# Optimization experiments

Hardware: AMD Instinct MI355X
Metric: run time of the kernel (lower is better)

The kernel has to match this reference:

```python
import jax, jax.numpy as jnp
import numpy as np

N = 8192        # batch_size == num nodes == num hyperedges
D = 512         # hidden_dim
H_HEADS = 8
HD = D // H_HEADS
TOP_K = 16
EPS = 1e-5      # LayerNorm eps


def setup_inputs() -> dict:
    key = jax.random.key(0)
    ks = jax.random.split(key, 10)
    def rn(k, shape, scale=0.02):
        return jax.random.normal(k, shape, dtype=jnp.float32) * scale
    return {
        "x0": jax.random.normal(ks[0], (N, D), dtype=jnp.float32),
        "x1": jax.random.normal(ks[1], (N, D), dtype=jnp.float32),
        # modality projections: Linear -> ReLU -> LayerNorm (per modality)
        "w_p0": rn(ks[2], (D, D)), "b_p0": jnp.zeros((D,), jnp.float32),
        "g0": jnp.ones((D,), jnp.float32), "beta0": jnp.zeros((D,), jnp.float32),
        "w_p1": rn(ks[3], (D, D)), "b_p1": jnp.zeros((D,), jnp.float32),
        "g1": jnp.ones((D,), jnp.float32), "beta1": jnp.zeros((D,), jnp.float32),
        # MultiheadAttention packed in-proj + out-proj
        "in_w": rn(ks[4], (3 * D, D)), "in_b": jnp.zeros((3 * D,), jnp.float32),
        "out_w": rn(ks[5], (D, D)), "out_b": jnp.zeros((D,), jnp.float32),
        # edge weight predictor MLP
        "ew_w1": rn(ks[6], (D // 2, D)), "ew_b1": jnp.zeros((D // 2,), jnp.float32),
        "ew_w2": rn(ks[7], (1, D // 2)), "ew_b2": jnp.zeros((1,), jnp.float32),
    }


def _layernorm(x, g, b):
    m = x.mean(-1, keepdims=True)
    v = ((x - m) ** 2).mean(-1, keepdims=True)
    return (x - m) * jax.lax.rsqrt(v + EPS) * g + b


def _forward(x0, x1, w_p0, b_p0, g0, beta0, w_p1, b_p1, g1, beta1,
             in_w, in_b, out_w, out_b, ew_w1, ew_b1, ew_w2, ew_b2):
    # per-modality projection: Linear -> ReLU -> LayerNorm
    p0 = _layernorm(jax.nn.relu(x0 @ w_p0.T + b_p0), g0, beta0)
    p1 = _layernorm(jax.nn.relu(x1 @ w_p1.T + b_p1), g1, beta1)
    seq = jnp.stack([p0, p1], axis=1)                       # [N, 2, D]
    # cross-modal MHA (self-attention over the 2 modality tokens)
    qkv = seq @ in_w.T + in_b                               # [N, 2, 3D]
    q, k, v = jnp.split(qkv, 3, axis=-1)
    q = q.reshape(N, 2, H_HEADS, HD)
    k = k.reshape(N, 2, H_HEADS, HD)
    v = v.reshape(N, 2, H_HEADS, HD)
    scores = jnp.einsum('bqhd,bkhd->bhqk', q, k) / jnp.sqrt(jnp.float32(HD))
    attn = jax.nn.softmax(scores, axis=-1)                  # [N, h, 2, 2]
    ctx = jnp.einsum('bhqk,bkhd->bqhd', attn, v).reshape(N, 2, D)
    attended = ctx @ out_w.T + out_b                        # [N, 2, D]
    fused = attended.mean(axis=1)                           # [N, D]
    # node-node attention similarity, row-softmax
    sim = jax.nn.softmax(fused @ fused.T, axis=1)           # [N, N]
    _, idx = jax.lax.top_k(sim, TOP_K)                      # [N, K]
    vals = jnp.take_along_axis(sim, idx, axis=1)            # [N, K]
    rows = jnp.arange(N)
    # H[i,i]=1 first, then H[neighbor, i] = sim[i, neighbor] (may overwrite diag)
    H = jnp.zeros((N, N), sim.dtype).at[rows, rows].set(1.0)
    H = H.at[idx, rows[:, None]].set(vals)
    colsum = H.sum(axis=0)
    H = H.at[rows, rows].set(jnp.where(colsum == 0, 1.0, H[rows, rows]))
    # edge weights
    hidden = jax.nn.relu(fused @ ew_w1.T + ew_b1)
    ew = jax.nn.sigmoid(hidden @ ew_w2.T + ew_b2)[:, 0]     # [N]
    ew = jnp.maximum(ew, 1e-8)
    return H, ew


def reference(x0, x1, w_p0, b_p0, g0, beta0, w_p1, b_p1, g1, beta1,
              in_w, in_b, out_w, out_b, ew_w1, ew_b1, ew_w2, ew_b2):
    return _forward(x0, x1, w_p0, b_p0, g0, beta0, w_p1, b_p1, g1, beta1,
                    in_w, in_b, out_w, out_b, ew_w1, ew_b1, ew_w2, ew_b2)
```

## Files before the change

### kernel.cpp

```cpp
#include <hip/hip_runtime.h>
#include <hip/hip_bf16.h>

#define NN 8192
#define DD 512

typedef unsigned short u16;
typedef __bf16 bf16_t;
typedef bf16_t bf16x8 __attribute__((ext_vector_type(8)));
typedef float f32x4 __attribute__((ext_vector_type(4)));

__device__ __forceinline__ float bf2f(u16 h) {
    union { unsigned u; float f; } v; v.u = ((unsigned)h) << 16; return v.f;
}
__device__ __forceinline__ float bflo(unsigned u) {
    union { unsigned u; float f; } v; v.u = u << 16; return v.f;
}
__device__ __forceinline__ float bfhi(unsigned u) {
    union { unsigned u; float f; } v; v.u = u & 0xFFFF0000u; return v.f;
}
__device__ __forceinline__ u16 f2bf(float f) {
    union { float f; unsigned u; } v; v.f = f;
    unsigned r = v.u + 0x7fffu + ((v.u >> 16) & 1u);
    return (u16)(r >> 16);
}

#define PIPE_BARRIER(N) do { \
    __builtin_amdgcn_sched_barrier(0); \
    asm volatile("s_waitcnt vmcnt(" #N ")" ::: "memory"); \
    __builtin_amdgcn_s_barrier(); \
    __builtin_amdgcn_sched_barrier(0); \
} while (0)

__global__ __launch_bounds__(256) void cvt5(
        const float* __restrict__ s0, u16* __restrict__ d0,
        const float* __restrict__ s1, u16* __restrict__ d1,
        const float* __restrict__ s2, u16* __restrict__ d2,
        const float* __restrict__ s3, u16* __restrict__ d3,
        const float* __restrict__ s4, u16* __restrict__ d4) {
    size_t v = ((size_t)blockIdx.x * 256 + threadIdx.x) * 8;
    const float* s; u16* d; size_t off;
    if (v < 262144)       { s = s0; d = d0; off = v; }
    else if (v < 524288)  { s = s1; d = d1; off = v - 262144; }
    else if (v < 1310720) { s = s2; d = d2; off = v - 524288; }
    else if (v < 1572864) { s = s3; d = d3; off = v - 1310720; }
    else                  { s = s4; d = d4; off = v - 1572864; }
    float4 a = *(const float4*)(s + off);
    float4 b = *(const float4*)(s + off + 4);
    ushort4 o0 = make_ushort4(f2bf(a.x), f2bf(a.y), f2bf(a.z), f2bf(a.w));
    ushort4 o1 = make_ushort4(f2bf(b.x), f2bf(b.y), f2bf(b.z), f2bf(b.w));
    *(ushort4*)(d + off) = o0;
    *(ushort4*)(d + off + 4) = o1;
}

#define EPS_LDS 136
__global__ __launch_bounds__(256) void gemm_proj(
        const float* __restrict__ X0, const float* __restrict__ X1,
        const u16* __restrict__ B0, const float* __restrict__ bias0,
        const u16* __restrict__ B1, const float* __restrict__ bias1,
        u16* __restrict__ C) {
    __shared__ alignas(16) u16 Smem[2][16384];
    const int t = threadIdx.x;
    const int lane = t & 63;
    const int wave = t >> 6;
    const int wm = (wave >> 1) * 64;
    const int wn = (wave & 1) * 64;
    const int rowA = blockIdx.y * 128;
    const int rowB = blockIdx.x * 128;
    const bool mod1 = (int)blockIdx.y >= 64;
    const float* A32 = mod1 ? X1 + (size_t)(rowA - 8192) * DD
                            : X0 + (size_t)rowA * DD;
    const u16* B = mod1 ? B1 : B0;
    const float* bias = mod1 ? bias1 : bias0;

    f32x4 acc[4][4] = {};
    const int mrow = lane & 15;
    const int kk = (lane >> 4) * 8;
    const int trow = t >> 3;
    const int koff = (t & 7) * 8;

    float ar[4][8];
    auto LOADA = [&](int k0) {
        #pragma unroll
        for (int r = 0; r < 4; ++r) {
            const float* s = A32 + (size_t)(r * 32 + trow) * DD + k0 + koff;
            float4 f0 = *(const float4*)s;
            float4 f1 = *(const float4*)(s + 4);
            ar[r][0] = f0.x; ar[r][1] = f0.y; ar[r][2] = f0.z; ar[r][3] = f0.w;
            ar[r][4] = f1.x; ar[r][5] = f1.y; ar[r][6] = f1.z; ar[r][7] = f1.w;
        }
    };
    auto WRITEA = [&](int buf) {
        u16* As = Smem[buf];
        #pragma unroll
        for (int r = 0; r < 4; ++r) {
            int chunk = r * 256 + t;
            ushort4 o0 = make_ushort4(f2bf(ar[r][0]), f2bf(ar[r][1]),
                                      f2bf(ar[r][2]), f2bf(ar[r][3]));
            ushort4 o1 = make_ushort4(f2bf(ar[r][4]), f2bf(ar[r][5]),
                                      f2bf(ar[r][6]), f2bf(ar[r][7]));
            *(ushort4*)(As + chunk * 8) = o0;
            *(ushort4*)(As + chunk * 8 + 4) = o1;
        }
    };
    auto BSTAGE = [&](int buf, int k0) {
        u16* Bs = Smem[buf] + 8192;
        #pragma unroll
        for (int r = 0; r < 4; ++r) {
            int chunk = r * 256 + t;
            const u16* srcB = B + (size_t)(rowB + (chunk >> 3)) * DD + k0 + (chunk & 7) * 8;
            __builtin_amdgcn_global_load_lds(
                (const __attribute__((address_space(1))) void*)srcB,
                (__attribute__((address_space(3))) void*)(Bs + chunk * 8), 16, 0, 0);
        }
    };

    LOADA(0); BSTAGE(0, 0); WRITEA(0);
    __syncthreads();
    int cur = 0;
    for (int ti = 0; ti < 8; ++ti) {
        if (ti < 7) { LOADA((ti + 1) << 6); BSTAGE(cur ^ 1, (ti + 1) << 6); }
        const u16* As = Smem[cur];
        const u16* Bs = Smem[cur] + 8192;
        #pragma unroll
        for (int ks = 0; ks < 64; ks += 32) {
            bf16x8 af[4], bfv[4];
            #pragma unroll
            for (int i = 0; i < 4; ++i)
                af[i] = *(const bf16x8*)(As + (wm + i * 16 + mrow) * 64 + ks + kk);
            #pragma unroll
            for (int j = 0; j < 4; ++j)
                bfv[j] = *(const bf16x8*)(Bs + (wn + j * 16 + mrow) * 64 + ks + kk);
            #pragma unroll
            for (int i = 0; i < 4; ++i)
                #pragma unroll
                for (int j = 0; j < 4; ++j)
                    acc[i][j] = __builtin_amdgcn_mfma_f32_16x16x32_bf16(af[i], bfv[j], acc[i][j], 0, 0, 0);
        }
        if (ti < 7) WRITEA(cur ^ 1);
        __syncthreads();
        cur ^= 1;
    }

    u16* Ep = &Smem[0][0];
    const int er0 = wm + (lane >> 4) * 4;
    const int ec0 = wn + (lane & 15);
    #pragma unroll
    for (int j = 0; j < 4; ++j) {
        int c = ec0 + j * 16;
        float bv = bias[rowB + c];
        #pragma unroll
        for (int i = 0; i < 4; ++i) {
            #pragma unroll
            for (int r = 0; r < 4; ++r) {
                float v = fmaxf(acc[i][j][r] + bv, 0.0f);
                Ep[(er0 + i * 16 + r) * EPS_LDS + c] = f2bf(v);
            }
        }
    }
    __syncthreads();
    #pragma unroll
    for (int pass = 0; pass < 8; ++pass) {
        int chunk = pass * 256 + t;
        int rloc = chunk >> 4, coff = (chunk & 15) * 8;
        bf16x8 v = *(const bf16x8*)(Ep + rloc * EPS_LDS + coff);
        *(bf16x8*)(C + (size_t)(rowA + rloc) * DD + rowB + coff) = v;
    }
}

__global__ __launch_bounds__(256) void gemm_qkv(const u16* __restrict__ A,
        const u16* __restrict__ B, const float* __restrict__ bias,
        u16* __restrict__ V, float* __restrict__ AL) {
    __shared__ alignas(16) u16 Smem[3][8192];
    const int t = threadIdx.x;
    const int lane = t & 63;
    const int wave = t >> 6;
    const int wm = (wave >> 1) * 64;
    const int wn = (wave & 1) * 64;
    const int c = blockIdx.x;
    const int rowA = blockIdx.y * 128;
    const bool isQK = (c < 8);

    f32x4 acc[4][4] = {};
    const int mrow = lane & 15;
    const int kk = (lane >> 4) * 8;

    auto STAGE = [&](int buf, int k0) {
        u16* As = Smem[buf];
        u16* Bs = Smem[buf] + 4096;
        #pragma unroll
        for (int r = 0; r < 2; ++r) {
            int chunk = r * 256 + t;
            int rr = chunk >> 2;
            int ko = (chunk & 3) * 8;
            int brow = isQK ? (c * 64 + rr + ((rr >= 64) ? 448 : 0))
                            : (1024 + (c - 8) * 128 + rr);
            const u16* srcA = A + (size_t)(rowA + rr) * DD + k0 + ko;
            __builtin_amdgcn_global_load_lds(
                (const __attribute__((address_space(1))) void*)srcA,
                (__attribute__((address_space(3))) void*)(As + chunk * 8), 16, 0, 0);
            const u16* srcB = B + (size_t)brow * DD + k0 + ko;
            __builtin_amdgcn_global_load_lds(
                (const __attribute__((address_space(1))) void*)srcB,
                (__attribute__((address_space(3))) void*)(Bs + chunk * 8), 16, 0, 0);
        }
    };
    auto COMPUTE = [&](int buf) {
        const u16* As = Smem[buf];
        const u16* Bs = Smem[buf] + 4096;
        bf16x8 af[4], bfv[4];
        #pragma unroll
        for (int i = 0; i < 4; ++i)
            af[i] = *(const bf16x8*)(As + (wm + i * 16 + mrow) * 32 + kk);
        #pragma unroll
        for (int j = 0; j < 4; ++j)
            bfv[j] = *(const bf16x8*)(Bs + (wn + j * 16 + mrow) * 32 + kk);
        #pragma unroll
        for (int i = 0; i < 4; ++i)
            #pragma unroll
            for (int j = 0; j < 4; ++j)
                acc[i][j] = __builtin_amdgcn_mfma_f32_16x16x32_bf16(af[i], bfv[j], acc[i][j], 0, 0, 0);
    };

    STAGE(0, 0);
    STAGE(1, 32);
    PIPE_BARRIER(4);
    #pragma unroll
    for (int ts = 0; ts < 14; ++ts) {
        STAGE((ts + 2) % 3, (ts + 2) * 32);
        COMPUTE(ts % 3);
        PIPE_BARRIER(4);
    }
    COMPUTE(2);
    PIPE_BARRIER(0);
    COMPUTE(0);
    __syncthreads();

    u16* Ep = &Smem[0][0];
    const int er0 = wm + (lane >> 4) * 4;
    const int ec0 = wn + (lane & 15);
    #pragma unroll
    for (int j = 0; j < 4; ++j) {
        int cc = ec0 + j * 16;
        int bcol = isQK ? ((cc < 64) ? c * 64 + cc : 448 + c * 64 + cc)
                        : (1024 + (c - 8) * 128 + cc);
        float bv = bias[bcol];
        #pragma unroll
        for (int i = 0; i < 4; ++i) {
            #pragma unroll
            for (int r = 0; r < 4; ++r)
                Ep[(er0 + i * 16 + r) * EPS_LDS + cc] = f2bf(acc[i][j][r] + bv);
        }
    }
    __syncthreads();
    if (isQK) {
        int nd = t >> 2, cb = t & 3, tt2 = cb >> 1, ss = cb & 1;
        const u16* qrow = Ep + (2 * nd + tt2) * EPS_LDS;
        const u16* krow = Ep + (2 * nd + ss) * EPS_LDS + 64;
        float s = 0.0f;
        #pragma unroll
        for (int d8 = 0; d8 < 8; ++d8) {
            bf16x8 qv = *(const bf16x8*)(qrow + d8 * 8);
            bf16x8 kv = *(const bf16x8*)(krow + d8 * 8);
            #pragma unroll
            for (int u = 0; u < 8; ++u) s += (float)qv[u] * (float)kv[u];
        }
        s *= 0.125f;
        float o = __shfl_xor(s, 1);
        float mm = fmaxf(s, o);
        float es = __expf(s - mm), eo = __expf(o - mm);
        float a = es / (es + eo);
        float a2 = __shfl_xor(a, 2);
        float al = 0.5f * (a + a2);
        if (cb < 2)
            AL[(size_t)(rowA / 2 + nd) * 16 + c * 2 + cb] = al;
    } else {
        #pragma unroll
        for (int pass = 0; pass < 8; ++pass) {
            int chunk = pass * 256 + t;
            int rloc = chunk >> 4, coff = (chunk & 15) * 8;
            bf16x8 v = *(const bf16x8*)(Ep + rloc * EPS_LDS + coff);
            *(bf16x8*)(V + (size_t)(rowA + rloc) * 512 + (c - 8) * 128 + coff) = v;
        }
    }
}

__global__ __launch_bounds__(256) void gemm_outp(
        const float* __restrict__ AL, const u16* __restrict__ V,
        const u16* __restrict__ W, const float* __restrict__ bias,
        u16* __restrict__ C) {
    __shared__ alignas(16) u16 Smem[2][16384];
    const int t = threadIdx.x;
    const int lane = t & 63;
    const int wave = t >> 6;
    const int wm = (wave >> 1) * 64;
    const int wn = (wave & 1) * 64;
    const int rowA = blockIdx.y * 128;
    const int rowB = blockIdx.x * 128;

    f32x4 acc[4][4] = {};
    const int mrow = lane & 15;
    const int kk = (lane >> 4) * 8;
    const int trow = t >> 3;
    const int koff = (t & 7) * 8;

    uint4 v0r[4], v1r[4];
    float2 alr[4];
    auto LOADA = [&](int ti) {
        #pragma unroll
        for (int r = 0; r < 4; ++r) {
            int node = rowA + r * 32 + trow;
            alr[r] = *(const float2*)(AL + (size_t)node * 16 + ti * 2);
            const u16* v0p = V + (size_t)(2 * node) * 512 + ti * 64 + koff;
            v0r[r] = *(const uint4*)v0p;
            v1r[r] = *(const uint4*)(v0p + 512);
        }
    };
    auto WRITEA = [&](int buf) {
        u16* As = Smem[buf];
        #pragma unroll
        for (int r = 0; r < 4; ++r) {
            int chunk = r * 256 + t;
            union { u16 us[8]; ushort4 u4[2]; } o;
            #pragma unroll
            for (int q = 0; q < 4; ++q) {
                unsigned w0 = (&v0r[r].x)[q], w1 = (&v1r[r].x)[q];
                o.us[q * 2]     = f2bf(alr[r].x * bflo(w0) + alr[r].y * bflo(w1));
                o.us[q * 2 + 1] = f2bf(alr[r].x * bfhi(w0) + alr[r].y * bfhi(w1));
            }
            *(ushort4*)(As + chunk * 8) = o.u4[0];
            *(ushort4*)(As + chunk * 8 + 4) = o.u4[1];
        }
    };
    auto BSTAGE = [&](int buf, int k0) {
        u16* Bs = Smem[buf] + 8192;
        #pragma unroll
        for (int r = 0; r < 4; ++r) {
            int chunk = r * 256 + t;
            const u16* srcB = W + (size_t)(rowB + (chunk >> 3)) * DD + k0 + (chunk & 7) * 8;
            __builtin_amdgcn_global_load_lds(
                (const __attribute__((address_space(1))) void*)srcB,
                (__attribute__((address_space(3))) void*)(Bs + chunk * 8), 16, 0, 0);
        }
    };

    LOADA(0); BSTAGE(0, 0); WRITEA(0);
    __syncthreads();
    int cur = 0;
    for (int ti = 0; ti < 8; ++ti) {
        if (ti < 7) { LOADA(ti + 1); BSTAGE(cur ^ 1, (ti + 1) << 6); }
        const u16* As = Smem[cur];
        const u16* Bs = Smem[cur] + 8192;
        #pragma unroll
        for (int ks = 0; ks < 64; ks += 32) {
            bf16x8 af[4], bfv[4];
            #pragma unroll
            for (int i = 0; i < 4; ++i)
                af[i] = *(const bf16x8*)(As + (wm + i * 16 + mrow) * 64 + ks + kk);
            #pragma unroll
            for (int j = 0; j < 4; ++j)
                bfv[j] = *(const bf16x8*)(Bs + (wn + j * 16 + mrow) * 64 + ks + kk);
            #pragma unroll
            for (int i = 0; i < 4; ++i)
                #pragma unroll
                for (int j = 0; j < 4; ++j)
                    acc[i][j] = __builtin_amdgcn_mfma_f32_16x16x32_bf16(af[i], bfv[j], acc[i][j], 0, 0, 0);
        }
        if (ti < 7) WRITEA(cur ^ 1);
        __syncthreads();
        cur ^= 1;
    }

    u16* Ep = &Smem[0][0];
    const int er0 = wm + (lane >> 4) * 4;
    const int ec0 = wn + (lane & 15);
    #pragma unroll
    for (int j = 0; j < 4; ++j) {
        int c = ec0 + j * 16;
        float bv = bias[rowB + c];
        #pragma unroll
        for (int i = 0; i < 4; ++i) {
            #pragma unroll
            for (int r = 0; r < 4; ++r)
                Ep[(er0 + i * 16 + r) * EPS_LDS + c] = f2bf(acc[i][j][r] + bv);
        }
    }
    __syncthreads();
    #pragma unroll
    for (int pass = 0; pass < 8; ++pass) {
        int chunk = pass * 256 + t;
        int rloc = chunk >> 4, coff = (chunk & 15) * 8;
        bf16x8 v = *(const bf16x8*)(Ep + rloc * EPS_LDS + coff);
        *(bf16x8*)(C + (size_t)(rowA + rloc) * DD + rowB + coff) = v;
    }
}

#define SYM_LDS 129
__global__ __launch_bounds__(256) void gemm_symh(const u16* __restrict__ F,
        u16* __restrict__ C, const u16* __restrict__ W1,
        const float* __restrict__ b1, u16* __restrict__ Hid) {
    __shared__ alignas(16) u16 Smem[3][8192];
    const int bx = blockIdx.x, by = blockIdx.y;
    const bool isHid = (bx >= 64);
    if (!isHid && bx < by) return;
    const int t = threadIdx.x;
    const int lane = t & 63;
    const int wave = t >> 6;
    const int wm = (wave >> 1) * 64;
    const int wn = (wave & 1) * 64;
    const int rowI = by * 128;
    const int rowJ = isHid ? (bx - 64) * 128 : bx * 128;
    const u16* Bsrc = isHid ? W1 : F;

    f32x4 acc[4][4] = {};
    const int mrow = lane & 15;
    const int kk = (lane >> 4) * 8;

    auto STAGE = [&](int buf, int k0) {
        u16* As = Smem[buf];
        u16* Bs = Smem[buf] + 4096;
        #pragma unroll
        for (int r = 0; r < 2; ++r) {
            int chunk = r * 256 + t;
            int row = chunk >> 2;
            int ko = (chunk & 3) * 8;
            const u16* srcA = F + (size_t)(rowI + row) * DD + k0 + ko;
            __builtin_amdgcn_global_load_lds(
                (const __attribute__((address_space(1))) void*)srcA,
                (__attribute__((address_space(3))) void*)(As + chunk * 8), 16, 0, 0);
            const u16* srcB = Bsrc + (size_t)(rowJ + row) * DD + k0 + ko;
            __builtin_amdgcn_global_load_lds(
                (const __attribute__((address_space(1))) void*)srcB,
                (__attribute__((address_space(3))) void*)(Bs + chunk * 8), 16, 0, 0);
        }
    };
    auto COMPUTE = [&](int buf) {
        const u16* As = Smem[buf];
        const u16* Bs = Smem[buf] + 4096;
        bf16x8 af[4], bfv[4];
        #pragma unroll
        for (int i = 0; i < 4; ++i)
            af[i] = *(const bf16x8*)(As + (wm + i * 16 + mrow) * 32 + kk);
        #pragma unroll
        for (int j = 0; j < 4; ++j)
            bfv[j] = *(const bf16x8*)(Bs + (wn + j * 16 + mrow) * 32 + kk);
        #pragma unroll
        for (int i = 0; i < 4; ++i)
            #pragma unroll
            for (int j = 0; j < 4; ++j)
                acc[i][j] = __builtin_amdgcn_mfma_f32_16x16x32_bf16(af[i], bfv[j], acc[i][j], 0, 0, 0);
    };

    STAGE(0, 0);
    STAGE(1, 32);
    PIPE_BARRIER(4);
    #pragma unroll
    for (int ts = 0; ts < 14; ++ts) {
        STAGE((ts + 2) % 3, (ts + 2) * 32);
        COMPUTE(ts % 3);
        PIPE_BARRIER(4);
    }
    COMPUTE(2);
    PIPE_BARRIER(0);
    COMPUTE(0);
    __syncthreads();

    u16* Ep = &Smem[0][0];
    const int er0 = wm + (lane >> 4) * 4;
    const int ec0 = wn + (lane & 15);
    #pragma unroll
    for (int j = 0; j < 4; ++j) {
        int c = ec0 + j * 16;
        float bv = isHid ? b1[rowJ + c] : 0.0f;
        #pragma unroll
        for (int i = 0; i < 4; ++i) {
            #pragma unroll
            for (int r = 0; r < 4; ++r) {
                float v = acc[i][j][r] + bv;
                if (isHid) v = fmaxf(v, 0.0f);
                Ep[(er0 + i * 16 + r) * SYM_LDS + c] = f2bf(v);
            }
        }
    }
    __syncthreads();
    if (isHid) {
        #pragma unroll
        for (int pass = 0; pass < 8; ++pass) {
            int chunk = pass * 256 + t;
            int rloc = chunk >> 4, coff = (chunk & 15) * 8;
            union { u16 us[8]; bf16x8 v; } buf;
            #pragma unroll
            for (int k = 0; k < 8; ++k) buf.us[k] = Ep[rloc * SYM_LDS + coff + k];
            *(bf16x8*)(Hid + (size_t)(rowI + rloc) * 256 + rowJ + coff) = buf.v;
        }
        return;
    }
    #pragma unroll
    for (int pass = 0; pass < 8; ++pass) {
        int chunk = pass * 256 + t;
        int rloc = chunk >> 4, coff = (chunk & 15) * 8;
        union { u16 us[8]; bf16x8 v; } buf;
        #pragma unroll
        for (int k = 0; k < 8; ++k) buf.us[k] = Ep[rloc * SYM_LDS + coff + k];
        *(bf16x8*)(C + (size_t)(rowI + rloc) * NN + rowJ + coff) = buf.v;
    }
    if (bx != by) {
        #pragma unroll
        for (int pass = 0; pass < 8; ++pass) {
            int chunk = pass * 256 + t;
            int tr = chunk >> 4, roff = (chunk & 15) * 8;
            union { u16 us[8]; bf16x8 v; } buf;
            #pragma unroll
            for (int k = 0; k < 8; ++k) buf.us[k] = Ep[(roff + k) * SYM_LDS + tr];
            *(bf16x8*)(C + (size_t)(rowJ + tr) * NN + rowI + roff) = buf.v;
        }
    }
}

__global__ __launch_bounds__(256) void ln2_kernel(const u16* __restrict__ y,
        const float* __restrict__ g0, const float* __restrict__ b0,
        const float* __restrict__ g1, const float* __restrict__ b1,
        u16* __restrict__ seq) {
    int n = blockIdx.x * 4 + (threadIdx.x >> 6);
    int lane = threadIdx.x & 63;
    int modality = n >> 13, node = n & (NN - 1);
    const float* g = modality ? g1 : g0;
    const float* b = modality ? b1 : b0;
    bf16x8 v = *(const bf16x8*)(y + (size_t)n * DD + lane * 8);
    float x[8];
    float s = 0.0f;
    #pragma unroll
    for (int u = 0; u < 8; ++u) { x[u] = (float)v[u]; s += x[u]; }
    #pragma unroll
    for (int off = 32; off; off >>= 1) s += __shfl_xor(s, off);
    float mean = s * (1.0f / DD);
    float vs = 0.0f;
    #pragma unroll
    for (int u = 0; u < 8; ++u) { x[u] -= mean; vs += x[u] * x[u]; }
    #pragma unroll
    for (int off = 32; off; off >>= 1) vs += __shfl_xor(vs, off);
    float inv = rsqrtf(vs * (1.0f / DD) + 1e-5f);
    float4 ga = *(const float4*)(g + lane * 8);
    float4 gb = *(const float4*)(g + lane * 8 + 4);
    float4 ba = *(const float4*)(b + lane * 8);
    float4 bb = *(const float4*)(b + lane * 8 + 4);
    union { u16 us[8]; bf16x8 v; } o;
    o.us[0] = f2bf(x[0] * inv * ga.x + ba.x);
    o.us[1] = f2bf(x[1] * inv * ga.y + ba.y);
    o.us[2] = f2bf(x[2] * inv * ga.z + ba.z);
    o.us[3] = f2bf(x[3] * inv * ga.w + ba.w);
    o.us[4] = f2bf(x[4] * inv * gb.x + bb.x);
    o.us[5] = f2bf(x[5] * inv * gb.y + bb.y);
    o.us[6] = f2bf(x[6] * inv * gb.z + bb.z);
    o.us[7] = f2bf(x[7] * inv * gb.w + bb.w);
    *(bf16x8*)(seq + (size_t)node * (2 * DD) + modality * DD + lane * 8) = o.v;
}

__global__ __launch_bounds__(256) void topk_bf16(u16* __restrict__ S,
        float* __restrict__ topv, int* __restrict__ topi,
        u16* __restrict__ hidden, const float* __restrict__ w2,
        const float* __restrict__ b2, float* __restrict__ ew_out,
        float* __restrict__ H) {
    const int blk = blockIdx.x;
    const int t = threadIdx.x;
    const float4 z4 = make_float4(0.f, 0.f, 0.f, 0.f);
    if (blk >= 2048) {
        int wv = t >> 6, lane = t & 63;
        int n0 = (blk - 2048) * 64 + wv * 16;
        float wa = w2[lane], wb = w2[lane + 64], wc = w2[lane + 128], wd = w2[lane + 192];
        for (int q = 0; q < 16; ++q) {
            int n = n0 + q;
            const u16* hr = hidden + (size_t)n * 256;
            float s = bf2f(hr[lane]) * wa + bf2f(hr[lane + 64]) * wb
                    + bf2f(hr[lane + 128]) * wc + bf2f(hr[lane + 192]) * wd;
            #pragma unroll
            for (int off = 32; off; off >>= 1) s += __shfl_xor(s, off);
            if (lane == 0) {
                float z = s + b2[0];
                float sig = 1.0f / (1.0f + __expf(-z));
                ew_out[n] = fmaxf(sig, 1e-8f);
            }
        }
        float4* zb = (float4*)(hidden + (size_t)n0 * 256);
        #pragma unroll
        for (int i = 0; i < 8; ++i) zb[i * 64 + lane] = z4;
        return;
    }
    const float NEG = -3e38f;
    const int SENT = 0x7FFFFFFF;
    int row = blk * 4 + (t >> 6);
    int lane = t & 63;
    u16* Sr = S + (size_t)row * NN;

    float m8[8], l8[8];
    #pragma unroll
    for (int k = 0; k < 8; ++k) { m8[k] = NEG; l8[k] = 0.0f; }
    float t1v = NEG, t2v = NEG, t3v = NEG;
    int t1i = SENT, t2i = SENT, t3i = SENT;

    #pragma unroll
    for (int p = 0; p < 16; ++p) {
        uint4 raw = *(const uint4*)(Sr + p * 512 + lane * 8);
        int base = p * 512 + lane * 8;
        #pragma unroll
        for (int q = 0; q < 4; ++q) {
            unsigned w = (&raw.x)[q];
            #pragma unroll
            for (int h = 0; h < 2; ++h) {
                float x = h ? bfhi(w) : bflo(w);
                int xi = base + q * 2 + h;
                int slot8 = q * 2 + h;
                if (x > m8[slot8]) {
                    l8[slot8] = l8[slot8] * __expf(m8[slot8] - x) + 1.0f;
                    m8[slot8] = x;
                } else l8[slot8] += __expf(x - m8[slot8]);
                bool g1 = x > t1v, g2 = x > t2v, g3 = x > t3v;
                t3v = g2 ? t2v : (g3 ? x : t3v);
                t3i = g2 ? t2i : (g3 ? xi : t3i);
                t2v = g1 ? t1v : (g2 ? x : t2v);
                t2i = g1 ? t1i : (g2 ? xi : t2i);
                t1v = g1 ? x : t1v;
                t1i = g1 ? xi : t1i;
            }
        }
    }
    float m = m8[0], l = l8[0];
    #pragma unroll
    for (int k = 1; k < 8; ++k) {
        float nm = fmaxf(m, m8[k]);
        l = l * __expf(m - nm) + l8[k] * __expf(m8[k] - nm);
        m = nm;
    }
    #pragma unroll
    for (int off = 32; off; off >>= 1) {
        float om = __shfl_xor(m, off);
        float ol = __shfl_xor(l, off);
        float nm = fmaxf(m, om);
        l = l * __expf(m - nm) + ol * __expf(om - nm);
        m = nm;
    }

    unsigned mk0 = 0, mk1 = 0, mk2 = 0, mk3 = 0;
    float c1v = t1v, c2v = t2v, c3v = t3v;
    int c1i = t1i, c2i = t2i, c3i = t3i;
    for (int r = 0; r < 16; ++r) {
        float wv = c1v; int wi = c1i;
        #pragma unroll
        for (int off = 32; off; off >>= 1) {
            float ov = __shfl_xor(wv, off);
            int oi = __shfl_xor(wi, off);
            if (ov > wv || (ov == wv && oi < wi)) { wv = ov; wi = oi; }
        }
        if (lane == 0) {
            topv[(size_t)row * 16 + r] = __expf(wv - m) / l;
            topi[(size_t)row * 16 + r] = wi;
        }
        if (wi == c1i) {
            int slot = ((wi >> 9) << 3) | (wi & 7);
            unsigned bit = 1u << (slot & 31);
            if (slot < 32) mk0 |= bit; else if (slot < 64) mk1 |= bit;
            else if (slot < 96) mk2 |= bit; else mk3 |= bit;
            c1v = c2v; c1i = c2i;
            c2v = c3v; c2i = c3i;
            c3v = NEG; c3i = SENT;
            if (c1i == SENT) {
                float nb = NEG; int ni = SENT;
                #pragma unroll
                for (int p = 0; p < 16; ++p) {
                    uint4 raw = *(const uint4*)(Sr + p * 512 + lane * 8);
                    int base = p * 512 + lane * 8;
                    #pragma unroll
                    for (int q = 0; q < 4; ++q) {
                        unsigned w = (&raw.x)[q];
                        #pragma unroll
                        for (int h = 0; h < 2; ++h) {
                            int sl = p * 8 + q * 2 + h;
                            unsigned mw = (sl < 32) ? mk0 : (sl < 64) ? mk1
                                        : (sl < 96) ? mk2 : mk3;
                            float x = ((mw >> (sl & 31)) & 1u) ? NEG
                                    : (h ? bfhi(w) : bflo(w));
                            if (x > nb) { nb = x; ni = base + q * 2 + h; }
                        }
                    }
                }
                c1v = nb; c1i = ni;
            }
        }
    }

    float4* srow = (float4*)Sr;
    #pragma unroll
    for (int i = 0; i < 16; ++i) srow[i * 64 + lane] = z4;

    {
        size_t vb0 = (size_t)blk * 63488;
        #pragma unroll
        for (int rr = 0; rr < 16; ++rr) {
            int j = rr * 256 + t;
            if (j < 3968) {
                size_t b = vb0 + (size_t)j * 16;
                char* p = (char*)H + (b < 109051904u ? b : b + 4194304u);
                *(float4*)p = z4;
            }
        }
    }
}

__global__ __launch_bounds__(256) void scatter_diag(const float* __restrict__ topv,
        const int* __restrict__ topi, float* __restrict__ H) {
    int tk = blockIdx.x * 256 + threadIdx.x;
    if (tk < NN * 16) {
        int i = tk >> 4;
        int idx = topi[tk];
        H[(size_t)idx * NN + i] = topv[tk];
    } else {
        int c = tk - NN * 16;
        const int* ti = topi + c * 16;
        bool self = false;
        #pragma unroll
        for (int j = 0; j < 16; ++j) self |= (ti[j] == c);
        if (!self) H[(size_t)c * NN + c] = 1.0f;
    }
}

extern "C" void kernel_launch(void* const* d_in, const int* in_sizes, int n_in,
                              void* d_out, int out_size, void* d_ws, size_t ws_size,
                              hipStream_t stream) {
    const float* x0    = (const float*)d_in[0];
    const float* x1    = (const float*)d_in[1];
    const float* w_p0  = (const float*)d_in[2];
    const float* b_p0  = (const float*)d_in[3];
    const float* g0    = (const float*)d_in[4];
    const float* beta0 = (const float*)d_in[5];
    const float* w_p1  = (const float*)d_in[6];
    const float* b_p1  = (const float*)d_in[7];
    const float* g1    = (const float*)d_in[8];
    const float* beta1 = (const float*)d_in[9];
    const float* in_w  = (const float*)d_in[10];
    const float* in_b  = (const float*)d_in[11];
    const float* out_w = (const float*)d_in[12];
    const float* out_b = (const float*)d_in[13];
    const float* ew_w1 = (const float*)d_in[14];
    const float* ew_b1 = (const float*)d_in[15];
    const float* ew_w2 = (const float*)d_in[16];
    const float* ew_b2 = (const float*)d_in[17];

    float* Hf = (float*)d_out;
    float* ew_out = Hf + (size_t)NN * NN;

    u16* Hu = (u16*)d_out;
    u16* y01    = Hu + 8388608;
    u16* seq    = Hu + 16777216;
    u16* Vbuf   = Hu + 25165824;
    u16* hidden = Hu + 54525952;
    float* ALb  = (float*)(Hu + 58720256);
    u16* wp0b   = Hu + 60817408;
    u16* wp1b   = wp0b + 262144;
    u16* inwb   = wp1b + 262144;
    u16* outwb  = inwb + 786432;
    u16* eww1b  = outwb + 262144;
    u16* Sb     = Hu + 67108864;
    char* ws = (char*)d_ws;
    u16* fusedB = (u16*)ws;
    float* topv = (float*)(ws + (8u << 20));
    int*   topi = (int*)(ws + (8u << 20) + 524288);

    dim3 blk(256);
    cvt5<<<dim3(832), blk, 0, stream>>>(w_p0, wp0b, w_p1, wp1b,
                                        in_w, inwb, out_w, outwb, ew_w1, eww1b);
    gemm_proj<<<dim3(4, 128), blk, 0, stream>>>(
        x0, x1, wp0b, b_p0, wp1b, b_p1, y01);
    ln2_kernel<<<dim3(2 * NN / 4), blk, 0, stream>>>(y01, g0, beta0, g1, beta1, seq);
    gemm_qkv<<<dim3(12, 128), blk, 0, stream>>>(seq, inwb, in_b, Vbuf, ALb);
    gemm_outp<<<dim3(4, 64), blk, 0, stream>>>(ALb, Vbuf, outwb, out_b, fusedB);
    gemm_symh<<<dim3(66, 64), blk, 0, stream>>>(fusedB, Sb, eww1b, ew_b1, hidden);
    topk_bf16<<<dim3(2176), blk, 0, stream>>>(Sb, topv, topi,
        hidden, ew_w2, ew_b2, ew_out, Hf);
    scatter_diag<<<dim3((NN * 16 + NN) / 256), blk, 0, stream>>>(topv, topi, Hf);
}
```

Baseline: 584.7 us.

## Enlarge symmetric similarity GEMM tiles to 256x256 with 512-thread blocks

The symmetric fused·fusedᵀ GEMM (plus the fused hidden-layer GEMM) now uses 256x256 output tiles computed by 8 waves of 512 threads, each wave holding a 128x64 accumulator. The epilogue is staged through LDS in two 128-row halves with a wider padded stride, and the non-transposed stores become direct 16-byte LDS reads. The intent is to raise arithmetic intensity, cut the per-tile global reloads and halve the number of blocks in the triangular grid. In exchange it uses more registers and LDS per block, which lowers occupancy, and leaves fewer blocks to spread across CUs.

Result: slower. 657.7 us (+12.5%).

```diff
diff --git a/kernel.cpp b/kernel.cpp
--- a/kernel.cpp
+++ b/kernel.cpp
@@ -394,33 +394,34 @@
     }
 }
 
-#define SYM_LDS 129
-__global__ __launch_bounds__(256) void gemm_symh(const u16* __restrict__ F,
+#define SEP 264
+__global__ __launch_bounds__(512) void gemm_symh(const u16* __restrict__ F,
         u16* __restrict__ C, const u16* __restrict__ W1,
         const float* __restrict__ b1, u16* __restrict__ Hid) {
-    __shared__ alignas(16) u16 Smem[3][8192];
+    __shared__ alignas(16) u16 Smem[3][16384];
     const int bx = blockIdx.x, by = blockIdx.y;
-    const bool isHid = (bx >= 64);
+    const bool isHid = (bx >= 32);
     if (!isHid && bx < by) return;
     const int t = threadIdx.x;
     const int lane = t & 63;
     const int wave = t >> 6;
-    const int wm = (wave >> 1) * 64;
-    const int wn = (wave & 1) * 64;
-    const int rowI = by * 128;
-    const int rowJ = isHid ? (bx - 64) * 128 : bx * 128;
+    const int wr = wave >> 2;
+    const int wc = wave & 3;
+    const int rowI = by * 256;
+    const int rowJ = isHid ? 0 : bx * 256;
     const u16* Bsrc = isHid ? W1 : F;
 
-    f32x4 acc[4][4] = {};
+    f32x4 acc[8][4] = {};
     const int mrow = lane & 15;
     const int kk = (lane >> 4) * 8;
 
-    auto STAGE = [&](int buf, int k0) {
+    auto STAGE = [&](int buf, int kt) {
+        int k0 = kt * 32;
         u16* As = Smem[buf];
-        u16* Bs = Smem[buf] + 4096;
+        u16* Bs = Smem[buf] + 8192;
         #pragma unroll
         for (int r = 0; r < 2; ++r) {
-            int chunk = r * 256 + t;
+            int chunk = r * 512 + t;
             int row = chunk >> 2;
             int ko = (chunk & 3) * 8;
             const u16* srcA = F + (size_t)(rowI + row) * DD + k0 + ko;
@@ -435,27 +436,27 @@
     };
     auto COMPUTE = [&](int buf) {
         const u16* As = Smem[buf];
-        const u16* Bs = Smem[buf] + 4096;
-        bf16x8 af[4], bfv[4];
-        #pragma unroll
-        for (int i = 0; i < 4; ++i)
-            af[i] = *(const bf16x8*)(As + (wm + i * 16 + mrow) * 32 + kk);
+        const u16* Bs = Smem[buf] + 8192;
+        bf16x8 af[8], bfv[4];
+        #pragma unroll
+        for (int i = 0; i < 8; ++i)
+            af[i] = *(const bf16x8*)(As + (wr * 128 + i * 16 + mrow) * 32 + kk);
         #pragma unroll
         for (int j = 0; j < 4; ++j)
-            bfv[j] = *(const bf16x8*)(Bs + (wn + j * 16 + mrow) * 32 + kk);
-        #pragma unroll
-        for (int i = 0; i < 4; ++i)
+            bfv[j] = *(const bf16x8*)(Bs + (wc * 64 + j * 16 + mrow) * 32 + kk);
+        #pragma unroll
+        for (int i = 0; i < 8; ++i)
             #pragma unroll
             for (int j = 0; j < 4; ++j)
                 acc[i][j] = __builtin_amdgcn_mfma_f32_16x16x32_bf16(af[i], bfv[j], acc[i][j], 0, 0, 0);
     };
 
     STAGE(0, 0);
-    STAGE(1, 32);
+    STAGE(1, 1);
     PIPE_BARRIER(4);
     #pragma unroll
     for (int ts = 0; ts < 14; ++ts) {
-        STAGE((ts + 2) % 3, (ts + 2) * 32);
+        STAGE((ts + 2) % 3, ts + 2);
         COMPUTE(ts % 3);
         PIPE_BARRIER(4);
     }
@@ -465,54 +466,55 @@
     __syncthreads();
 
     u16* Ep = &Smem[0][0];
-    const int er0 = wm + (lane >> 4) * 4;
-    const int ec0 = wn + (lane & 15);
-    #pragma unroll
-    for (int j = 0; j < 4; ++j) {
-        int c = ec0 + j * 16;
-        float bv = isHid ? b1[rowJ + c] : 0.0f;
-        #pragma unroll
-        for (int i = 0; i < 4; ++i) {
-            #pragma unroll
-            for (int r = 0; r < 4; ++r) {
-                float v = acc[i][j][r] + bv;
-                if (isHid) v = fmaxf(v, 0.0f);
-                Ep[(er0 + i * 16 + r) * SYM_LDS + c] = f2bf(v);
-            }
-        }
-    }
-    __syncthreads();
-    if (isHid) {
-        #pragma unroll
-        for (int pass = 0; pass < 8; ++pass) {
-            int chunk = pass * 256 + t;
-            int rloc = chunk >> 4, coff = (chunk & 15) * 8;
-            union { u16 us[8]; bf16x8 v; } buf;
-            #pragma unroll
-            for (int k = 0; k < 8; ++k) buf.us[k] = Ep[rloc * SYM_LDS + coff + k];
-            *(bf16x8*)(Hid + (size_t)(rowI + rloc) * 256 + rowJ + coff) = buf.v;
-        }
-        return;
-    }
-    #pragma unroll
-    for (int pass = 0; pass < 8; ++pass) {
-        int chunk = pass * 256 + t;
-        int rloc = chunk >> 4, coff = (chunk & 15) * 8;
-        union { u16 us[8]; bf16x8 v; } buf;
-        #pragma unroll
-        for (int k = 0; k < 8; ++k) buf.us[k] = Ep[rloc * SYM_LDS + coff + k];
-        *(bf16x8*)(C + (size_t)(rowI + rloc) * NN + rowJ + coff) = buf.v;
-    }
-    if (bx != by) {
-        #pragma unroll
-        for (int pass = 0; pass < 8; ++pass) {
-            int chunk = pass * 256 + t;
-            int tr = chunk >> 4, roff = (chunk & 15) * 8;
-            union { u16 us[8]; bf16x8 v; } buf;
-            #pragma unroll
-            for (int k = 0; k < 8; ++k) buf.us[k] = Ep[(roff + k) * SYM_LDS + tr];
-            *(bf16x8*)(C + (size_t)(rowJ + tr) * NN + rowI + roff) = buf.v;
-        }
+    #pragma unroll
+    for (int h = 0; h < 2; ++h) {
+        if (wr == h) {
+            #pragma unroll
+            for (int j = 0; j < 4; ++j) {
+                int c = wc * 64 + j * 16 + (lane & 15);
+                float bv = isHid ? b1[c] : 0.0f;
+                #pragma unroll
+                for (int i = 0; i < 8; ++i) {
+                    #pragma unroll
+                    for (int r = 0; r < 4; ++r) {
+                        float v = acc[i][j][r] + bv;
+                        if (isHid) v = fmaxf(v, 0.0f);
+                        Ep[(i * 16 + (lane >> 4) * 4 + r) * SEP + c] = f2bf(v);
+                    }
+                }
+            }
+        }
+        __syncthreads();
+        if (isHid) {
+            #pragma unroll
+            for (int pass = 0; pass < 8; ++pass) {
+                int chunk = pass * 512 + t;
+                int rloc = chunk >> 5, coff = (chunk & 31) * 8;
+                bf16x8 v = *(const bf16x8*)(Ep + rloc * SEP + coff);
+                *(bf16x8*)(Hid + (size_t)(rowI + h * 128 + rloc) * 256 + coff) = v;
+            }
+        } else {
+            #pragma unroll
+            for (int pass = 0; pass < 8; ++pass) {
+                int chunk = pass * 512 + t;
+                int rloc = chunk >> 5, coff = (chunk & 31) * 8;
+                bf16x8 v = *(const bf16x8*)(Ep + rloc * SEP + coff);
+                *(bf16x8*)(C + (size_t)(rowI + h * 128 + rloc) * NN + rowJ + coff) = v;
+            }
+            if (bx != by) {
+                #pragma unroll
+                for (int pass = 0; pass < 8; ++pass) {
+                    int chunk = pass * 512 + t;
+                    int tr = chunk >> 4, roff = (chunk & 15) * 8;
+                    union { u16 us[8]; bf16x8 v; } buf;
+                    #pragma unroll
+                    for (int k = 0; k < 8; ++k)
+                        buf.us[k] = Ep[(roff + k) * SEP + tr];
+                    *(bf16x8*)(C + (size_t)(rowJ + tr) * NN + rowI + h * 128 + roff) = buf.v;
+                }
+            }
+        }
+        __syncthreads();
     }
 }
 
@@ -772,7 +774,7 @@
     ln2_kernel<<<dim3(2 * NN / 4), blk, 0, stream>>>(y01, g0, beta0, g1, beta1, seq);
     gemm_qkv<<<dim3(12, 128), blk, 0, stream>>>(seq, inwb, in_b, Vbuf, ALb);
     gemm_outp<<<dim3(4, 64), blk, 0, stream>>>(ALb, Vbuf, outwb, out_b, fusedB);
-    gemm_symh<<<dim3(66, 64), blk, 0, stream>>>(fusedB, Sb, eww1b, ew_b1, hidden);
+    gemm_symh<<<dim3(33, 32), dim3(512), 0, stream>>>(fusedB, Sb, eww1b, ew_b1, hidden);
     topk_bf16<<<dim3(2176), blk, 0, stream>>>(Sb, topv, topi,
         hidden, ew_w2, ew_b2, ew_out, Hf);
     scatter_diag<<<dim3((NN * 16 + NN) / 256), blk, 0, stream>>>(topv, topi, Hf);
```
